# Kernel optimization log

Hardware: AMD Instinct MI355X
Metric: run time of the kernel (lower is better)

## Reference

```python
import jax, jax.numpy as jnp
import numpy as np

TEMPERATURE = 0.07
EPS = 1e-8  # torch CosineSimilarity eps


def setup_inputs() -> dict:
    key = jax.random.key(0)
    k1, k2 = jax.random.split(key)
    B, D = 4096, 256
    z_i = jax.random.normal(k1, (B, D), dtype=jnp.float32)
    z_j = jax.random.normal(k2, (B, D), dtype=jnp.float32)
    return {"z_i": z_i, "z_j": z_j}


def reference(z_i, z_j):
    B = z_j.shape[0]
    z = jnp.concatenate([z_i, z_j], axis=0)  # [2B, D]
    # normalize_hidden=True: F.normalize(p=2, dim=-1)
    z = z / jnp.maximum(jnp.linalg.norm(z, axis=-1, keepdims=True), 1e-12)
    # CosineSimilarity(dim=2) on unsqueezed tensors == row-normalized Gram matrix.
    # (rows already unit-norm, so this second normalization matches torch's cosine sim)
    zn = z / jnp.maximum(jnp.linalg.norm(z, axis=-1, keepdims=True), EPS)
    sim = jnp.einsum("nd,md->nm", zn, zn) / TEMPERATURE  # [2B, 2B]
    # positives: diag(sim, +B) and diag(sim, -B)
    pos = jnp.concatenate([jnp.diagonal(sim, offset=B), jnp.diagonal(sim, offset=-B)])  # [2B]
    # negatives: all off-diagonal entries per row (positive pair included, as in original)
    offdiag = 1.0 - jnp.eye(2 * B, dtype=sim.dtype)
    neg_sum = jnp.sum(jnp.exp(sim) * offdiag, axis=-1)  # [2B]
    # -log(exp(pos) / neg_sum) = log(neg_sum) - pos
    loss = jnp.mean(jnp.log(neg_sum) - pos)
    return loss
```

## Files before the change

kernel.cpp:

```cpp
#include <hip/hip_runtime.h>
#include <hip/hip_bf16.h>

typedef __attribute__((ext_vector_type(4))) float f32x4;
typedef __attribute__((ext_vector_type(2))) long i64x2;

typedef const __attribute__((address_space(1))) void* gptr_t;
typedef __attribute__((address_space(3))) void* lptr_t;

#define NROW 8192
#define DDIM 256
#define HALF_B 4096
#define NB 64
#define NTILES (NB * (NB + 1) / 2)

#define E2SCALE 20.6099291555566196f
#define INV_T   14.2857142857142858f

__device__ __forceinline__ float fast_exp2(float x) {
  float r;
  asm("v_exp_f32 %0, %1" : "=v"(r) : "v"(x));
  return r;
}

__global__ __launch_bounds__(256) void normalize_kernel(
    const float* __restrict__ z_i, const float* __restrict__ z_j,
    unsigned char* __restrict__ zn, float* __restrict__ lacc,
    unsigned int* __restrict__ counter) {
  const int lane = threadIdx.x & 63;
  const int w = blockIdx.x * 4 + (threadIdx.x >> 6);
  const int g  = (lane >> 1) & 3;
  const int e  = (lane >> 3) & 1;
  const int ph = (lane >> 4) & 1;
  const int pq = lane >> 5;
  const int o  = (lane & 1) * 4;
  const int cbase = (ph << 2) | g;
  for (int row = w; row < NROW; row += 2048) {
    const float* src = (row < HALF_B) ? (z_i + (size_t)row * DDIM)
                                      : (z_j + (size_t)(row - HALF_B) * DDIM);
    float4 v = *reinterpret_cast<const float4*>(src + lane * 4);
    float ss = v.x * v.x + v.y * v.y + v.z * v.z + v.w * v.w;
#pragma unroll
    for (int m = 32; m; m >>= 1) ss += __shfl_xor(ss, m);
    const float inv = 1.0f / sqrtf(ss);
    int pk = __builtin_amdgcn_cvt_pk_fp8_f32(v.x * inv, v.y * inv, 0, false);
    pk = __builtin_amdgcn_cvt_pk_fp8_f32(v.z * inv, v.w * inv, pk, true);
    const int pos = pq * 128 + ((cbase ^ (row & 7)) << 4) + e * 8 + o;
    *reinterpret_cast<unsigned int*>(zn + (size_t)row * DDIM + pos) =
        (unsigned int)pk;
  }
  if (blockIdx.x == 0 && threadIdx.x == 0) { *lacc = 0.0f; *counter = 0u; }
}

__global__ __launch_bounds__(256, 4) void gram_kernel(
    const unsigned char* __restrict__ zn,
    float* __restrict__ P, float* __restrict__ pos) {
  __shared__ char smem[33792];
  float (*colmat)[2] = (float (*)[2])(smem + 32768);

  const int tid = threadIdx.x;
  const int lane = tid & 63;
  const int wid = tid >> 6;
  const int wr = wid >> 1;
  const int wc = wid & 1;

  int p = blockIdx.x;
  int by = 0;
  while (p >= NB - by) { p -= NB - by; ++by; }
  const int bx = by + p;
  const int rowBase = by * 128;
  const int colBase = bx * 128;
  const bool isdiag = (bx == by);
  const bool ispos = (bx - by == 32);

  const int rloc = tid >> 3;
  const int c16 = (tid & 7) * 16;
  const int r15 = lane & 15, g = lane >> 4, r7 = lane & 7;
  const int abase = (wr * 64 + r15) * 128;
  const int bbase = (wc * 64 + r15) * 128;

  f32x4 acc[4][4] = {};

#pragma unroll
  for (int h = 0; h < 2; ++h) {
#pragma unroll
    for (int i = 0; i < 4; ++i) {
      const int r = i * 32 + rloc;
      const unsigned char* ga =
          zn + (size_t)(rowBase + r) * DDIM + h * 128 + c16;
      __builtin_amdgcn_global_load_lds((gptr_t)ga,
          (lptr_t)(smem + i * 4096 + wid * 1024), 16, 0, 0);
    }
#pragma unroll
    for (int i = 0; i < 4; ++i) {
      const int r = i * 32 + rloc;
      const unsigned char* gb =
          zn + (size_t)(colBase + r) * DDIM + h * 128 + c16;
      __builtin_amdgcn_global_load_lds((gptr_t)gb,
          (lptr_t)(smem + 16384 + i * 4096 + wid * 1024), 16, 0, 0);
    }
    asm volatile("s_waitcnt vmcnt(0)" ::: "memory");
    __builtin_amdgcn_s_barrier();
    __builtin_amdgcn_sched_barrier(0);

    const char* Ab = reinterpret_cast<const char*>(smem);
    const char* Bb = reinterpret_cast<const char*>(smem) + 16384;
#pragma unroll
    for (int lp = 0; lp < 2; ++lp) {
      const int off = ((((lp << 2) | g) ^ r7) << 4);
      i64x2 A0 = *reinterpret_cast<const i64x2*>(Ab + abase + off);
      i64x2 A1 = *reinterpret_cast<const i64x2*>(Ab + abase + 2048 + off);
      i64x2 A2 = *reinterpret_cast<const i64x2*>(Ab + abase + 4096 + off);
      i64x2 A3 = *reinterpret_cast<const i64x2*>(Ab + abase + 6144 + off);
      i64x2 B0 = *reinterpret_cast<const i64x2*>(Bb + bbase + off);
      i64x2 B1 = *reinterpret_cast<const i64x2*>(Bb + bbase + 2048 + off);
      i64x2 B2 = *reinterpret_cast<const i64x2*>(Bb + bbase + 4096 + off);
      i64x2 B3 = *reinterpret_cast<const i64x2*>(Bb + bbase + 6144 + off);
#pragma unroll
      for (int e = 0; e < 2; ++e) {
        const long a[4] = {A0[e], A1[e], A2[e], A3[e]};
        const long b[4] = {B0[e], B1[e], B2[e], B3[e]};
#pragma unroll
        for (int m = 0; m < 4; ++m)
#pragma unroll
          for (int n = 0; n < 4; ++n)
            acc[m][n] = __builtin_amdgcn_mfma_f32_16x16x32_fp8_fp8(
                a[m], b[n], acc[m][n], 0, 0, 0);
      }
    }
    __syncthreads();
  }

  char* rowm = smem;
  float colpart[4] = {0.0f, 0.0f, 0.0f, 0.0f};
  const int slot = wc * 16 + r15;
#pragma unroll
  for (int m = 0; m < 4; ++m) {
#pragma unroll
    for (int v = 0; v < 4; ++v) {
      const int lrow = wr * 64 + m * 16 + (lane >> 4) * 4 + v;
      const int gi = rowBase + lrow;
      float rp = 0.0f;
#pragma unroll
      for (int n = 0; n < 4; ++n) {
        const float d = acc[m][n][v];
        float val = fast_exp2(d * E2SCALE);
        if (isdiag) {
          const int gj = colBase + wc * 64 + n * 16 + r15;
          if (gi == gj) val = 0.0f;
        } else if (ispos) {
          const int gj = colBase + wc * 64 + n * 16 + r15;
          if (gj == gi + HALF_B) {
            const float pv = d * INV_T;
            pos[gi] = pv;
            pos[gj] = pv;
          }
        }
        rp += val;
        colpart[n] += val;
      }
      const int bo = (lrow << 8) + ((((slot >> 2) ^ (lrow & 15)) << 4)) +
                     ((slot & 3) << 2);
      *reinterpret_cast<float*>(rowm + bo) = rp;
    }
  }
#pragma unroll
  for (int n = 0; n < 4; ++n) {
    float c = colpart[n];
    c += __shfl_xor(c, 16);
    c += __shfl_xor(c, 32);
    if (lane < 16) colmat[wc * 64 + n * 16 + lane][wr] = c;
  }
  __syncthreads();

  {
    const int row = tid >> 1;
    const int half = tid & 1;
    f32x4 s4 = {0.0f, 0.0f, 0.0f, 0.0f};
#pragma unroll
    for (int i = 0; i < 4; ++i) {
      const int c = half * 4 + i;
      s4 += *reinterpret_cast<const f32x4*>(
          rowm + (row << 8) + ((c ^ (row & 15)) << 4));
    }
    float s = (s4[0] + s4[1]) + (s4[2] + s4[3]);
    s += __shfl_xor(s, 1);
    if (half == 0) P[(size_t)bx * NROW + rowBase + row] = s;
  }
  if (tid < 128 && !isdiag) {
    P[(size_t)by * NROW + colBase + tid] = colmat[tid][0] + colmat[tid][1];
  }
}

__global__ __launch_bounds__(256) void rowreduce_kernel(
    const float* __restrict__ P, const float* __restrict__ pos,
    float* __restrict__ lacc, unsigned int* __restrict__ counter,
    float* __restrict__ out) {
  const int i = blockIdx.x * 256 + threadIdx.x;
  float s = 0.0f;
#pragma unroll 8
  for (int k = 0; k < NB; ++k) s += P[(size_t)k * NROW + i];
  float partial = logf(s) - pos[i];
#pragma unroll
  for (int m = 32; m; m >>= 1) partial += __shfl_xor(partial, m);
  __shared__ float sred[4];
  if ((threadIdx.x & 63) == 0) sred[threadIdx.x >> 6] = partial;
  __syncthreads();
  if (threadIdx.x == 0) {
    atomicAdd(lacc, sred[0] + sred[1] + sred[2] + sred[3]);
    __threadfence();
    const unsigned done = atomicAdd(counter, 1u);
    if (done == (unsigned)(gridDim.x - 1)) {
      const float v = atomicAdd(lacc, 0.0f);
      out[0] = v * (1.0f / (float)NROW);
    }
  }
}

extern "C" void kernel_launch(void* const* d_in, const int* in_sizes, int n_in,
                              void* d_out, int out_size, void* d_ws, size_t ws_size,
                              hipStream_t stream) {
  const float* z_i = (const float*)d_in[0];
  const float* z_j = (const float*)d_in[1];
  float* out = (float*)d_out;

  char* ws = (char*)d_ws;
  unsigned char* zn = (unsigned char*)ws;
  float* pos  = (float*)(ws + 2097152);
  float* P    = (float*)(ws + 2097152 + 32768);
  float* lacc = (float*)(ws + 2097152 + 32768 + 2097152);
  unsigned int* counter = (unsigned int*)(ws + 2097152 + 32768 + 2097152 + 4);

  normalize_kernel<<<512, 256, 0, stream>>>(z_i, z_j, zn, lacc, counter);
  gram_kernel<<<NTILES, 256, 0, stream>>>(zn, P, pos);
  rowreduce_kernel<<<NROW / 256, 256, 0, stream>>>(P, pos, lacc, counter, out);
}
```

Before: 36.09 us.

## Overlap second K-half load with MFMA and remap tile order across XCDs

The gram kernel now issues the global-to-LDS load for the second K half while the MFMAs of the first half's second slice run. All LDS reads are completed and a barrier is taken before the buffer is overwritten, which removes one full load-wait bubble per tile. The block index is also permuted so that consecutive tiles on the same XCD share rows, aiming for better L2 locality. This adds extra barriers and waitcnts, and the permutation depends on the tile count (2080 = 8*260).

```diff
diff --git a/kernel.cpp b/kernel.cpp
--- a/kernel.cpp
+++ b/kernel.cpp
@@ -63,7 +63,7 @@
   const int wr = wid >> 1;
   const int wc = wid & 1;
 
-  int p = blockIdx.x;
+  int p = (blockIdx.x & 7) * 260 + (blockIdx.x >> 3);
   int by = 0;
   while (p >= NB - by) { p -= NB - by; ++by; }
   const int bx = by + p;
@@ -78,10 +78,7 @@
   const int abase = (wr * 64 + r15) * 128;
   const int bbase = (wc * 64 + r15) * 128;
 
-  f32x4 acc[4][4] = {};
-
-#pragma unroll
-  for (int h = 0; h < 2; ++h) {
+  auto stage = [&](int h) {
 #pragma unroll
     for (int i = 0; i < 4; ++i) {
       const int r = i * 32 + rloc;
@@ -98,15 +95,30 @@
       __builtin_amdgcn_global_load_lds((gptr_t)gb,
           (lptr_t)(smem + 16384 + i * 4096 + wid * 1024), 16, 0, 0);
     }
-    asm volatile("s_waitcnt vmcnt(0)" ::: "memory");
-    __builtin_amdgcn_s_barrier();
-    __builtin_amdgcn_sched_barrier(0);
-
+  };
+
+  f32x4 acc[4][4] = {};
+
+  auto mfma16 = [&](const long* a, const long* b) {
+#pragma unroll
+    for (int m = 0; m < 4; ++m)
+#pragma unroll
+      for (int n = 0; n < 4; ++n)
+        acc[m][n] = __builtin_amdgcn_mfma_f32_16x16x32_fp8_fp8(
+            a[m], b[n], acc[m][n], 0, 0, 0);
+  };
+
+  stage(0);
+  asm volatile("s_waitcnt vmcnt(0)" ::: "memory");
+  __builtin_amdgcn_s_barrier();
+  __builtin_amdgcn_sched_barrier(0);
+
+#pragma unroll
+  for (int h = 0; h < 2; ++h) {
     const char* Ab = reinterpret_cast<const char*>(smem);
     const char* Bb = reinterpret_cast<const char*>(smem) + 16384;
-#pragma unroll
-    for (int lp = 0; lp < 2; ++lp) {
-      const int off = ((((lp << 2) | g) ^ r7) << 4);
+    {
+      const int off = ((g ^ r7) << 4);
       i64x2 A0 = *reinterpret_cast<const i64x2*>(Ab + abase + off);
       i64x2 A1 = *reinterpret_cast<const i64x2*>(Ab + abase + 2048 + off);
       i64x2 A2 = *reinterpret_cast<const i64x2*>(Ab + abase + 4096 + off);
@@ -119,15 +131,38 @@
       for (int e = 0; e < 2; ++e) {
         const long a[4] = {A0[e], A1[e], A2[e], A3[e]};
         const long b[4] = {B0[e], B1[e], B2[e], B3[e]};
-#pragma unroll
-        for (int m = 0; m < 4; ++m)
-#pragma unroll
-          for (int n = 0; n < 4; ++n)
-            acc[m][n] = __builtin_amdgcn_mfma_f32_16x16x32_fp8_fp8(
-                a[m], b[n], acc[m][n], 0, 0, 0);
-      }
-    }
-    __syncthreads();
+        mfma16(a, b);
+      }
+    }
+    {
+      const int off = (((4 | g) ^ r7) << 4);
+      i64x2 A0 = *reinterpret_cast<const i64x2*>(Ab + abase + off);
+      i64x2 A1 = *reinterpret_cast<const i64x2*>(Ab + abase + 2048 + off);
+      i64x2 A2 = *reinterpret_cast<const i64x2*>(Ab + abase + 4096 + off);
+      i64x2 A3 = *reinterpret_cast<const i64x2*>(Ab + abase + 6144 + off);
+      i64x2 B0 = *reinterpret_cast<const i64x2*>(Bb + bbase + off);
+      i64x2 B1 = *reinterpret_cast<const i64x2*>(Bb + bbase + 2048 + off);
+      i64x2 B2 = *reinterpret_cast<const i64x2*>(Bb + bbase + 4096 + off);
+      i64x2 B3 = *reinterpret_cast<const i64x2*>(Bb + bbase + 6144 + off);
+      asm volatile("s_waitcnt lgkmcnt(0)" ::: "memory");
+      __builtin_amdgcn_sched_barrier(0);
+      __builtin_amdgcn_s_barrier();
+      if (h == 0) {
+        stage(1);
+        __builtin_amdgcn_sched_barrier(0);
+      }
+#pragma unroll
+      for (int e = 0; e < 2; ++e) {
+        const long a[4] = {A0[e], A1[e], A2[e], A3[e]};
+        const long b[4] = {B0[e], B1[e], B2[e], B3[e]};
+        mfma16(a, b);
+      }
+      if (h == 0) {
+        asm volatile("s_waitcnt vmcnt(0)" ::: "memory");
+        __builtin_amdgcn_s_barrier();
+        __builtin_amdgcn_sched_barrier(0);
+      }
+    }
   }
 
   char* rowm = smem;
```

Result: slower. 37.01 us (+2.5%).
